# Kernel tuning notes

Measured on AMD Instinct MI355X. Metric: run time of the kernel, lower is better.

The kernel has to match this reference:

```python
import jax, jax.numpy as jnp
import numpy as np
from jax import lax

N, T, IN = 64, 1024, 64
H = 512
H2 = H // 2   # 256
H4 = H // 4   # 128
H10 = H // 10 # 51


def _lstm(x, Wih, Whh, bih, bhh):
    """PyTorch-style LSTM, batch_first. x: [N,T,in]. Returns hs [N,T,h], h_T, c_T."""
    n, t, _ = x.shape
    h = Whh.shape[1]
    b = bih + bhh

    def step(carry, xt):
        hprev, cprev = carry
        gates = xt @ Wih.T + hprev @ Whh.T + b
        i, f, g, o = jnp.split(gates, 4, axis=-1)
        i = jax.nn.sigmoid(i)
        f = jax.nn.sigmoid(f)
        g = jnp.tanh(g)
        o = jax.nn.sigmoid(o)
        c = f * cprev + i * g
        hnew = o * jnp.tanh(c)
        return (hnew, c), hnew

    h0 = jnp.zeros((n, h), x.dtype)
    c0 = jnp.zeros((n, h), x.dtype)
    (hT, cT), hs = lax.scan(step, (h0, c0), x.transpose(1, 0, 2))
    return hs.transpose(1, 0, 2), hT, cT


def _causal_self_attention(hs):
    """Unscaled dot-product causal attention, equivalent to the python loop."""
    n, t, h = hs.shape
    scores = jnp.einsum('nth,nsh->nts', hs, hs)  # [N,T,T]
    mask = jnp.tril(jnp.ones((t, t), bool))
    scores = jnp.where(mask[None], scores, -jnp.inf)
    attn = jax.nn.softmax(scores, axis=-1)
    return jnp.einsum('nts,nsh->nth', attn, hs)


def setup_inputs() -> dict:
    key = jax.random.key(0)
    ks = jax.random.split(key, 16)
    s = 0.05
    return {
        'x': jax.random.normal(ks[0], (N, T, IN), jnp.float32),
        'W_ih1': jax.random.normal(ks[1], (4 * H, IN), jnp.float32) * s,
        'W_hh1': jax.random.normal(ks[2], (4 * H, H), jnp.float32) * s,
        'b_ih1': jax.random.normal(ks[3], (4 * H,), jnp.float32) * s,
        'b_hh1': jax.random.normal(ks[4], (4 * H,), jnp.float32) * s,
        'W_ih2': jax.random.normal(ks[5], (4 * H2, H), jnp.float32) * s,
        'W_hh2': jax.random.normal(ks[6], (4 * H2, H2), jnp.float32) * s,
        'b_ih2': jax.random.normal(ks[7], (4 * H2,), jnp.float32) * s,
        'b_hh2': jax.random.normal(ks[8], (4 * H2,), jnp.float32) * s,
        'fc1_w': jax.random.normal(ks[9], (H4, 2 * H2), jnp.float32) * s,
        'fc1_b': jax.random.normal(ks[10], (H4,), jnp.float32) * s,
        'fc2_w': jax.random.normal(ks[11], (H10, H4), jnp.float32) * s,
        'fc2_b': jax.random.normal(ks[12], (H10,), jnp.float32) * s,
        'fc3_w': jax.random.normal(ks[13], (1, H10), jnp.float32) * s,
        'fc3_b': jax.random.normal(ks[14], (1,), jnp.float32) * s,
    }


def reference(x, W_ih1, W_hh1, b_ih1, b_hh1, W_ih2, W_hh2, b_ih2, b_hh2,
              fc1_w, fc1_b, fc2_w, fc2_b, fc3_w, fc3_b):
    out, h1, c1 = _lstm(x, W_ih1, W_hh1, b_ih1, b_hh1)     # [N,T,H]
    out, h2, c2 = _lstm(out, W_ih2, W_hh2, b_ih2, b_hh2)   # [N,T,H2]
    contexts = _causal_self_attention(out)                  # [N,T,H2]
    out = jnp.concatenate((contexts, out), axis=2)          # [N,T,2*H2]
    out = jax.nn.relu(out @ fc1_w.T + fc1_b)                # dropout_ratio=0 -> identity
    out = jax.nn.relu(out @ fc2_w.T + fc2_b)
    out = out @ fc3_w.T + fc3_b                              # [N,T,1]
    return out, h1, c1, h2, c2
```

## Files before the change

kernel.cpp:

```cpp
#include <hip/hip_runtime.h>
#include <hip/hip_bf16.h>

#define N_   64
#define T_   1024
#define IN_  64
#define H1_  512
#define H2_  256
#define NG   4
#define NU1  16
#define NU2  8
#define RING 8
#define RING2 4
#define SENT 0xAAAAAAAAu

typedef __bf16 bf16x8 __attribute__((ext_vector_type(8)));
typedef float  f32x4  __attribute__((ext_vector_type(4)));
typedef unsigned int u32x4 __attribute__((ext_vector_type(4)));
typedef unsigned short u16x8 __attribute__((ext_vector_type(8)));
typedef unsigned long long u64;
typedef __hip_bfloat16 bf16_t;

#define OFF_FLG2  8192u
#define OFF_QUE   12288u
#define ZERO_BYTES 16384u
#define OFF_H1R   16384u
#define OFF_H2R   540672u
#define OFF_XB    671744u
#define OFF_W1    9060352u
#define OFF_W2    11419648u
#define OFF_B1    12992512u
#define OFF_B2    13000704u
#define OFF_FC1W  13004800u
#define OFF_FC2W  13135872u
#define OFF_HS2   13152256u
#define OFF_BURN  46706688u

__device__ __forceinline__ bf16x8 ld16(const bf16_t* p) {
  u32x4 u = *reinterpret_cast<const u32x4*>(p);
  return __builtin_bit_cast(bf16x8, u);
}
__device__ __forceinline__ u64 ld64_mall(const void* p) {
  return __hip_atomic_load((const u64*)p, __ATOMIC_RELAXED, __HIP_MEMORY_SCOPE_AGENT);
}
__device__ __forceinline__ void st4_mall(bf16_t* p, unsigned v) {
  __hip_atomic_store((unsigned*)p, v, __ATOMIC_RELAXED, __HIP_MEMORY_SCOPE_AGENT);
}
__device__ __forceinline__ unsigned ldflag(unsigned* p) {
  return __hip_atomic_load(p, __ATOMIC_RELAXED, __HIP_MEMORY_SCOPE_AGENT);
}
__device__ __forceinline__ bool sentok(u64 w) {
  return ((unsigned)w != SENT) && ((unsigned)(w >> 32) != SENT);
}
__device__ __forceinline__ f32x4 mfma_bf16(bf16x8 a, bf16x8 b, f32x4 c) {
  return __builtin_amdgcn_mfma_f32_16x16x32_bf16(a, b, c, 0, 0, 0);
}
__device__ __forceinline__ float sigf(float x) { return 1.f / (1.f + __expf(-x)); }
__device__ __forceinline__ float tanh_fast(float x) {
  float e = __expf(-2.f * fabsf(x));
  float r = (1.f - e) / (1.f + e);
  return x < 0.f ? -r : r;
}
__device__ __forceinline__ unsigned short bf16_bits(float v) {
  __hip_bfloat16 b = __float2bfloat16(v);
  return *reinterpret_cast<unsigned short*>(&b);
}

__global__ void setup_kernel(const float* __restrict__ x,
    const float* __restrict__ Wih1, const float* __restrict__ Whh1,
    const float* __restrict__ bih1, const float* __restrict__ bhh1,
    const float* __restrict__ Wih2, const float* __restrict__ Whh2,
    const float* __restrict__ bih2, const float* __restrict__ bhh2,
    const float* __restrict__ fc1w, const float* __restrict__ fc2w,
    char* __restrict__ ws)
{
  bf16_t* xb = (bf16_t*)(ws + OFF_XB);
  bf16_t* w1 = (bf16_t*)(ws + OFF_W1);
  bf16_t* w2 = (bf16_t*)(ws + OFF_W2);
  float*  b1 = (float*)(ws + OFF_B1);
  float*  b2 = (float*)(ws + OFF_B2);
  bf16_t* f1 = (bf16_t*)(ws + OFF_FC1W);
  bf16_t* f2 = (bf16_t*)(ws + OFF_FC2W);
  const long E0 = 4194304, E1 = E0 + 1179648, E2 = E1 + 786432,
             E3 = E2 + 2048, E4 = E3 + 1024, E5 = E4 + 65536, E6 = E5 + 8192;
  for (long i = blockIdx.x * (long)blockDim.x + threadIdx.x; i < E6;
       i += (long)gridDim.x * blockDim.x) {
    if (i < E0) {
      xb[i] = __float2bfloat16(x[i]);
    } else if (i < E1) {
      long idx = i - E0; long j = idx / 576, k = idx % 576;
      float v = (k < 64) ? Wih1[j * 64 + k] : Whh1[j * 512 + (k - 64)];
      w1[idx] = __float2bfloat16(v);
    } else if (i < E2) {
      long idx = i - E1; long j = idx / 768, k = idx % 768;
      float v = (k < 512) ? Wih2[j * 512 + k] : Whh2[j * 256 + (k - 512)];
      w2[idx] = __float2bfloat16(v);
    } else if (i < E3) {
      long idx = i - E2; b1[idx] = bih1[idx] + bhh1[idx];
    } else if (i < E4) {
      long idx = i - E3; b2[idx] = bih2[idx] + bhh2[idx];
    } else if (i < E5) {
      long idx = i - E4; f1[idx] = __float2bfloat16(fc1w[idx]);
    } else {
      long idx = i - E5; long j = idx / 128, k = idx % 128;
      f2[idx] = __float2bfloat16(j < 51 ? fc2w[j * 128 + k] : 0.f);
    }
  }
}

__global__ __launch_bounds__(256, 1) void fused_kernel(char* __restrict__ ws,
    const float* __restrict__ fc1b, const float* __restrict__ fc2b,
    const float* __restrict__ fc3w, const float* __restrict__ fc3b,
    float* __restrict__ dout)
{
  const bf16_t* xb  = (const bf16_t*)(ws + OFF_XB);
  const bf16_t* W1  = (const bf16_t*)(ws + OFF_W1);
  const bf16_t* W2  = (const bf16_t*)(ws + OFF_W2);
  const float*  b1  = (const float*)(ws + OFF_B1);
  const float*  b2  = (const float*)(ws + OFF_B2);
  bf16_t* h1r = (bf16_t*)(ws + OFF_H1R);
  bf16_t* h2r = (bf16_t*)(ws + OFF_H2R);
  bf16_t* hs2 = (bf16_t*)(ws + OFF_HS2);
  unsigned* flag2 = (unsigned*)(ws + OFF_FLG2);

  __shared__ __align__(16) char smem[55296];

  const int tid  = threadIdx.x;
  const int wave = tid >> 6;
  const int lane = tid & 63;
  const int l15  = lane & 15;
  const int quad = lane >> 4;
  const int bx   = blockIdx.x;
  const f32x4 z = {0.f, 0.f, 0.f, 0.f};

  if (bx < NG * NU1) {
    const int g = bx >> 4, u = bx & 15, u0 = u * 32;
    bf16_t* hstage = (bf16_t*)smem;
    float*  gbuf   = (float*)(smem + 18688);
    bf16x8 wf[18][2];
    #pragma unroll
    for (int i = 0; i < 18; ++i)
      #pragma unroll
      for (int nt = 0; nt < 2; ++nt)
        wf[i][nt] = ld16(W1 + (size_t)(wave * H1_ + u0 + nt * 16 + l15) * 576 + i * 32 + quad * 8);

    const int sr = tid >> 4;
    const int myp = tid & 15;
    const int row = tid >> 4, ui = (tid & 15) * 2;
    const int nrow = g * 16 + row;
    unsigned* bp = flag2 + (g * NU2 + (tid & 7)) * 32;
    float bi[2], bff[2], bg[2], bo[2], creg[2];
    #pragma unroll
    for (int j = 0; j < 2; ++j) {
      int ug = u0 + ui + j;
      bi[j]  = b1[ug];         bff[j] = b1[H1_ + ug];
      bg[j]  = b1[2*H1_ + ug]; bo[j]  = b1[3*H1_ + ug];
      creg[j] = 0.f;
    }
    #pragma unroll
    for (int s = 0; s < RING; ++s)
      st4_mall(h1r + ((size_t)(g * RING + s) * 16 + row) * 512 + u0 + ui, SENT);

    #pragma unroll 1
    for (int t = 0; t < T_; ++t) {
      {
        u64 xv = *(const u64*)(xb + ((size_t)(g*16 + sr) * T_ + t) * IN_ + myp * 4);
        *(u64*)(hstage + sr * 584 + myp * 4) = xv;
      }
      if (t >= 7)
        while ((int)ldflag(bp) < t - 6) __builtin_amdgcn_s_sleep(1);
      if (t == 0) {
        #pragma unroll
        for (int k = 0; k < 8; ++k)
          *(u64*)(hstage + sr * 584 + 64 + myp * 32 + k * 4) = 0ull;
      } else {
        const u64* src = (const u64*)(h1r + ((size_t)(g * RING + ((t-1) & 7)) * 16 + sr) * 512 + myp * 32);
        u64 w[8];
        for (;;) {
          #pragma unroll
          for (int k = 0; k < 8; ++k) w[k] = ld64_mall(src + k);
          bool ok = true;
          #pragma unroll
          for (int k = 0; k < 8; ++k) ok &= sentok(w[k]);
          if (ok) break;
          __builtin_amdgcn_s_sleep(1);
        }
        #pragma unroll
        for (int k = 0; k < 8; ++k)
          *(u64*)(hstage + sr * 584 + 64 + myp * 32 + k * 4) = w[k];
      }
      __syncthreads();
      st4_mall(h1r + ((size_t)(g * RING + ((t+1) & 7)) * 16 + row) * 512 + u0 + ui, SENT);
      f32x4 acc[2] = {z, z};
      #pragma unroll
      for (int ki = 0; ki < 18; ++ki) {
        bf16x8 aw = ld16(hstage + l15 * 584 + ki * 32 + quad * 8);
        acc[0] = mfma_bf16(aw, wf[ki][0], acc[0]);
        acc[1] = mfma_bf16(aw, wf[ki][1], acc[1]);
      }
      #pragma unroll
      for (int nt = 0; nt < 2; ++nt)
        #pragma unroll
        for (int r = 0; r < 4; ++r)
          gbuf[(wave * 16 + quad * 4 + r) * 33 + nt * 16 + l15] = acc[nt][r];
      __syncthreads();
      {
        unsigned pack = 0;
        float hv[2];
        #pragma unroll
        for (int j = 0; j < 2; ++j) {
          int col = ui + j;
          float iv = sigf(gbuf[(0*16 + row) * 33 + col] + bi[j]);
          float fv = sigf(gbuf[(1*16 + row) * 33 + col] + bff[j]);
          float gv = tanh_fast(gbuf[(2*16 + row) * 33 + col] + bg[j]);
          float ov = sigf(gbuf[(3*16 + row) * 33 + col] + bo[j]);
          float c = fv * creg[j] + iv * gv;
          creg[j] = c;
          float h = ov * tanh_fast(c);
          hv[j] = h;
          pack |= (unsigned)bf16_bits(h) << (16 * j);
        }
        st4_mall(h1r + ((size_t)(g * RING + (t & 7)) * 16 + row) * 512 + u0 + ui, pack);
        if (t == T_ - 1) {
          #pragma unroll
          for (int j = 0; j < 2; ++j) {
            dout[65536 + nrow * H1_ + u0 + ui + j] = hv[j];
            dout[98304 + nrow * H1_ + u0 + ui + j] = creg[j];
          }
        }
      }
    }
  } else if (bx < NG * NU1 + NG * NU2) {
    const int b2x = bx - NG * NU1;
    const int g = b2x >> 3, u = b2x & 7, u0 = u * 32;
    bf16_t* hstage = (bf16_t*)smem;
    float*  gbuf   = (float*)(smem + 25088);
    bf16x8 wf[24][2];
    #pragma unroll
    for (int i = 0; i < 24; ++i)
      #pragma unroll
      for (int nt = 0; nt < 2; ++nt)
        wf[i][nt] = ld16(W2 + (size_t)(wave * H2_ + u0 + nt * 16 + l15) * 768 + i * 32 + quad * 8);

    const int sr = tid >> 4;
    const int q  = tid & 15;
    const int row = tid >> 4, ui = (tid & 15) * 2;
    const int nrow = g * 16 + row;
    float bi[2], bff[2], bg[2], bo[2], creg[2];
    #pragma unroll
    for (int j = 0; j < 2; ++j) {
      int ug = u0 + ui + j;
      bi[j]  = b2[ug];         bff[j] = b2[H2_ + ug];
      bg[j]  = b2[2*H2_ + ug]; bo[j]  = b2[3*H2_ + ug];
      creg[j] = 0.f;
    }
    #pragma unroll
    for (int s = 0; s < RING2; ++s)
      st4_mall(h2r + ((size_t)(g * RING2 + s) * 16 + row) * 256 + u0 + ui, SENT);

    #pragma unroll 1
    for (int t = 0; t < T_; ++t) {
      {
        const u64* s1 = (const u64*)(h1r + ((size_t)(g * RING + (t & 7)) * 16 + sr) * 512 + q * 32);
        u64 w[8];
        for (;;) {
          #pragma unroll
          for (int k = 0; k < 8; ++k) w[k] = ld64_mall(s1 + k);
          bool ok = true;
          #pragma unroll
          for (int k = 0; k < 8; ++k) ok &= sentok(w[k]);
          if (ok) break;
          __builtin_amdgcn_s_sleep(1);
        }
        #pragma unroll
        for (int k = 0; k < 8; ++k)
          *(u64*)(hstage + sr * 784 + q * 32 + k * 4) = w[k];
      }
      if (t == 0) {
        #pragma unroll
        for (int k = 0; k < 4; ++k)
          *(u64*)(hstage + sr * 784 + 512 + q * 16 + k * 4) = 0ull;
      } else {
        const u64* s2 = (const u64*)(h2r + ((size_t)(g * RING2 + ((t-1) & 3)) * 16 + sr) * 256 + q * 16);
        u64 w[4];
        for (;;) {
          #pragma unroll
          for (int k = 0; k < 4; ++k) w[k] = ld64_mall(s2 + k);
          bool ok = true;
          #pragma unroll
          for (int k = 0; k < 4; ++k) ok &= sentok(w[k]);
          if (ok) break;
          __builtin_amdgcn_s_sleep(1);
        }
        #pragma unroll
        for (int k = 0; k < 4; ++k)
          *(u64*)(hstage + sr * 784 + 512 + q * 16 + k * 4) = w[k];
      }
      __syncthreads();
      st4_mall(h2r + ((size_t)(g * RING2 + ((t+1) & 3)) * 16 + row) * 256 + u0 + ui, SENT);
      f32x4 acc[2] = {z, z};
      #pragma unroll
      for (int ki = 0; ki < 24; ++ki) {
        bf16x8 aw = ld16(hstage + l15 * 784 + ki * 32 + quad * 8);
        acc[0] = mfma_bf16(aw, wf[ki][0], acc[0]);
        acc[1] = mfma_bf16(aw, wf[ki][1], acc[1]);
      }
      #pragma unroll
      for (int nt = 0; nt < 2; ++nt)
        #pragma unroll
        for (int r = 0; r < 4; ++r)
          gbuf[(wave * 16 + quad * 4 + r) * 33 + nt * 16 + l15] = acc[nt][r];
      __syncthreads();
      {
        unsigned pack = 0;
        float hv[2];
        #pragma unroll
        for (int j = 0; j < 2; ++j) {
          int col = ui + j;
          float iv = sigf(gbuf[(0*16 + row) * 33 + col] + bi[j]);
          float fv = sigf(gbuf[(1*16 + row) * 33 + col] + bff[j]);
          float gv = tanh_fast(gbuf[(2*16 + row) * 33 + col] + bg[j]);
          float ov = sigf(gbuf[(3*16 + row) * 33 + col] + bo[j]);
          float c = fv * creg[j] + iv * gv;
          creg[j] = c;
          float h = ov * tanh_fast(c);
          hv[j] = h;
          pack |= (unsigned)bf16_bits(h) << (16 * j);
        }
        st4_mall(h2r + ((size_t)(g * RING2 + (t & 3)) * 16 + row) * 256 + u0 + ui, pack);
        st4_mall(hs2 + ((size_t)nrow * T_ + t) * H2_ + u0 + ui, pack);
        if (t == T_ - 1) {
          #pragma unroll
          for (int j = 0; j < 2; ++j) {
            dout[131072 + nrow * H2_ + u0 + ui + j] = hv[j];
            dout[147456 + nrow * H2_ + u0 + ui + j] = creg[j];
          }
        }
      }
      __syncthreads();
      if (tid == 0)
        __hip_atomic_store(flag2 + (g * NU2 + u) * 32, (unsigned)(t + 1),
                           __ATOMIC_RELAXED, __HIP_MEMORY_SCOPE_AGENT);
    }
  }

  __syncthreads();
  {
    const bf16_t* f1w = (const bf16_t*)(ws + OFF_FC1W);
    const bf16_t* f2w = (const bf16_t*)(ws + OFF_FC2W);
    unsigned* queue = (unsigned*)(ws + OFF_QUE);
    unsigned short* vtile = (unsigned short*)smem;
    bf16_t* plds   = (bf16_t*)(smem + 36864);
    bf16_t* ctxlds = (bf16_t*)smem;
    bf16_t* act1   = (bf16_t*)(smem + 36864);
    float*  act2   = (float*)smem;
    volatile int* itemslot = (volatile int*)(smem + 55040);
    float burn = 1.0f;

    for (;;) {
      if (tid == 0) *itemslot = (int)atomicAdd(queue, 1u);
      __syncthreads();
      const int item = *itemslot;
      __syncthreads();
      if (item >= 1024) break;
      const int qt = item >> 6, n = item & 63, q0 = qt * 64, gg = n >> 4;

      {
        const int need = q0 + 64;
        if (tid < 64) {
          unsigned* p = (lane < NU2) ? flag2 + (gg * NU2 + lane) * 32 : nullptr;
          bool ok = (p == nullptr) || ((int)ldflag(p) >= need);
          while (!__all(ok)) {
            #pragma unroll
            for (int k = 0; k < 32; ++k) burn = fmaf(burn, 1.0000001f, 1e-7f);
            ok = (p == nullptr) || ((int)ldflag(p) >= need);
          }
        }
        __syncthreads();
      }

      bf16x8 aq[8];
      #pragma unroll
      for (int ks = 0; ks < 8; ++ks)
        aq[ks] = ld16(hs2 + ((size_t)n * T_ + q0 + wave * 16 + l15) * H2_ + ks * 32 + quad * 8);
      f32x4 o[16];
      #pragma unroll
      for (int ct = 0; ct < 16; ++ct) o[ct] = z;
      float m_run[4], l_run[4];
      #pragma unroll
      for (int r = 0; r < 4; ++r) { m_run[r] = -1e30f; l_run[r] = 0.f; }
      bf16_t* pw = plds + wave * 1152;

      #pragma unroll 1
      for (int st = 0; st <= qt; ++st) {
        const int s0 = st * 64;
        __syncthreads();
        #pragma unroll
        for (int it = 0; it < 8; ++it) {
          int s  = (tid >> 3) + (it & 1) * 32;
          int c0 = (tid & 7) * 8 + (it >> 1) * 64;
          u16x8 v = *reinterpret_cast<const u16x8*>(
              (const unsigned short*)hs2 + ((size_t)n * T_ + s0 + s) * H2_ + c0);
          #pragma unroll
          for (int j = 0; j < 8; ++j) {
            int ch = c0 + j;
            int sw = (s & 7) | ((((s >> 3) ^ (ch >> 3)) & 7) << 3);
            vtile[ch * 72 + sw] = v[j];
          }
        }
        __syncthreads();
        f32x4 sc[4] = {z, z, z, z};
        #pragma unroll
        for (int ks = 0; ks < 8; ++ks) {
          #pragma unroll
          for (int nt = 0; nt < 4; ++nt) {
            bf16x8 bk = ld16(hs2 + ((size_t)n * T_ + s0 + nt * 16 + l15) * H2_ + ks * 32 + quad * 8);
            sc[nt] = mfma_bf16(aq[ks], bk, sc[nt]);
          }
        }
        if (st == qt) {
          int qg = q0 + wave * 16 + quad * 4;
          #pragma unroll
          for (int nt = 0; nt < 4; ++nt) {
            int sg = s0 + nt * 16 + l15;
            #pragma unroll
            for (int r = 0; r < 4; ++r)
              if (sg > qg + r) sc[nt][r] = -1e30f;
          }
        }
        float alpha[4];
        #pragma unroll
        for (int r = 0; r < 4; ++r) {
          float tm = fmaxf(fmaxf(sc[0][r], sc[1][r]), fmaxf(sc[2][r], sc[3][r]));
          tm = fmaxf(tm, __shfl_xor(tm, 1, 16));
          tm = fmaxf(tm, __shfl_xor(tm, 2, 16));
          tm = fmaxf(tm, __shfl_xor(tm, 4, 16));
          tm = fmaxf(tm, __shfl_xor(tm, 8, 16));
          float mnew = fmaxf(m_run[r], tm);
          alpha[r] = __expf(m_run[r] - mnew);
          m_run[r] = mnew;
          float ts = 0.f;
          #pragma unroll
          for (int nt = 0; nt < 4; ++nt) {
            float p = __expf(sc[nt][r] - mnew);
            sc[nt][r] = p;
            ts += p;
          }
          ts += __shfl_xor(ts, 1, 16);
          ts += __shfl_xor(ts, 2, 16);
          ts += __shfl_xor(ts, 4, 16);
          ts += __shfl_xor(ts, 8, 16);
          l_run[r] = l_run[r] * alpha[r] + ts;
        }
        #pragma unroll
        for (int ct = 0; ct < 16; ++ct)
          #pragma unroll
          for (int r = 0; r < 4; ++r)
            o[ct][r] *= alpha[r];
        #pragma unroll
        for (int nt = 0; nt < 4; ++nt)
          #pragma unroll
          for (int r = 0; r < 4; ++r)
            pw[(quad * 4 + r) * 72 + nt * 16 + l15] = __float2bfloat16(sc[nt][r]);
        #pragma unroll
        for (int ks2 = 0; ks2 < 2; ++ks2) {
          bf16x8 ap = ld16(pw + l15 * 72 + ks2 * 32 + quad * 8);
          #pragma unroll
          for (int ct = 0; ct < 16; ++ct) {
            int ch = ct * 16 + l15;
            int blk = ((ks2 * 4 + quad) ^ (ch >> 3)) & 7;
            bf16x8 bv = ld16((bf16_t*)vtile + ch * 72 + blk * 8);
            o[ct] = mfma_bf16(ap, bv, o[ct]);
          }
        }
      }
      __syncthreads();
      float inv[4];
      #pragma unroll
      for (int r = 0; r < 4; ++r) inv[r] = 1.f / l_run[r];
      #pragma unroll
      for (int ct = 0; ct < 16; ++ct)
        #pragma unroll
        for (int r = 0; r < 4; ++r)
          ctxlds[(wave * 16 + quad * 4 + r) * 264 + ct * 16 + l15] =
              __float2bfloat16(o[ct][r] * inv[r]);
      __syncthreads();

      f32x4 a1[4][2];
      #pragma unroll
      for (int mt = 0; mt < 4; ++mt) { a1[mt][0] = z; a1[mt][1] = z; }
      #pragma unroll
      for (int ks = 0; ks < 16; ++ks) {
        bf16x8 af[4];
        if (ks < 8) {
          #pragma unroll
          for (int mt = 0; mt < 4; ++mt)
            af[mt] = ld16(ctxlds + (mt * 16 + l15) * 264 + ks * 32 + quad * 8);
        } else {
          #pragma unroll
          for (int mt = 0; mt < 4; ++mt)
            af[mt] = ld16(hs2 + ((size_t)n * T_ + q0 + mt * 16 + l15) * H2_ + (ks - 8) * 32 + quad * 8);
        }
        #pragma unroll
        for (int nt = 0; nt < 2; ++nt) {
          bf16x8 bw = ld16(f1w + (size_t)(wave * 32 + nt * 16 + l15) * 512 + ks * 32 + quad * 8);
          #pragma unroll
          for (int mt = 0; mt < 4; ++mt)
            a1[mt][nt] = mfma_bf16(af[mt], bw, a1[mt][nt]);
        }
      }
      #pragma unroll
      for (int mt = 0; mt < 4; ++mt)
        #pragma unroll
        for (int nt = 0; nt < 2; ++nt)
          #pragma unroll
          for (int r = 0; r < 4; ++r) {
            int ch = wave * 32 + nt * 16 + l15;
            float v = a1[mt][nt][r] + fc1b[ch];
            act1[(mt * 16 + quad * 4 + r) * 136 + ch] = __float2bfloat16(fmaxf(v, 0.f));
          }
      __syncthreads();

      f32x4 a2[4] = {z, z, z, z};
      #pragma unroll
      for (int ks = 0; ks < 4; ++ks) {
        bf16x8 bw = ld16(f2w + (wave * 16 + l15) * 128 + ks * 32 + quad * 8);
        #pragma unroll
        for (int mt = 0; mt < 4; ++mt) {
          bf16x8 af = ld16(act1 + (mt * 16 + l15) * 136 + ks * 32 + quad * 8);
          a2[mt] = mfma_bf16(af, bw, a2[mt]);
        }
      }
      __syncthreads();
      #pragma unroll
      for (int mt = 0; mt < 4; ++mt)
        #pragma unroll
        for (int r = 0; r < 4; ++r) {
          int ch = wave * 16 + l15;
          int rw = mt * 16 + quad * 4 + r;
          float v = a2[mt][r] + (ch < 51 ? fc2b[ch] : 0.f);
          act2[rw * 68 + ch] = fmaxf(v, 0.f);
        }
      __syncthreads();
      if (tid < 64) {
        float s = fc3b[0];
        for (int c = 0; c < 51; ++c) s += act2[tid * 68 + c] * fc3w[c];
        dout[(size_t)n * T_ + q0 + tid] = s;
      }
      __syncthreads();
    }
    if (burn == 0.1234567f)
      ((float*)(ws + OFF_BURN))[tid] = burn;
  }
}

extern "C" void kernel_launch(void* const* d_in, const int* in_sizes, int n_in,
                              void* d_out, int out_size, void* d_ws, size_t ws_size,
                              hipStream_t stream) {
  (void)in_sizes; (void)n_in; (void)out_size; (void)ws_size;
  const float* x    = (const float*)d_in[0];
  const float* Wih1 = (const float*)d_in[1];
  const float* Whh1 = (const float*)d_in[2];
  const float* bih1 = (const float*)d_in[3];
  const float* bhh1 = (const float*)d_in[4];
  const float* Wih2 = (const float*)d_in[5];
  const float* Whh2 = (const float*)d_in[6];
  const float* bih2 = (const float*)d_in[7];
  const float* bhh2 = (const float*)d_in[8];
  const float* fc1w = (const float*)d_in[9];
  const float* fc1b = (const float*)d_in[10];
  const float* fc2w = (const float*)d_in[11];
  const float* fc2b = (const float*)d_in[12];
  const float* fc3w = (const float*)d_in[13];
  const float* fc3b = (const float*)d_in[14];
  char* ws  = (char*)d_ws;
  float* out = (float*)d_out;

  hipMemsetAsync(ws, 0, ZERO_BYTES, stream);
  setup_kernel<<<2048, 256, 0, stream>>>(x, Wih1, Whh1, bih1, bhh1,
                                         Wih2, Whh2, bih2, bhh2, fc1w, fc2w, ws);
  fused_kernel<<<256, 256, 0, stream>>>(ws, fc1b, fc2b, fc3w, fc3b, out);
}
```

Measured before the change: 3.182 ms.

## Prefetch next h1 slice, split MFMA chains, drop spin sleeps, move flag publish

Layer-2 blocks now speculatively load the next timestep's h1 ring slice at the end of each step and only re-poll if sentinels are still present. The flag2 publish moves to right after the staging barrier, signalling step t-1 consumed, and the trailing __syncthreads per step is removed. Both LSTM layers split the MFMA accumulation into two independent chains to cut dependency latency, and the s_sleep in spin loops is dropped to react faster. The changes shorten the serial per-step critical path. In exchange, the sleep-free spinning adds memory traffic, and the reordered flag and barrier protocol risks ring-reuse races.

```diff
diff --git a/kernel.cpp b/kernel.cpp
--- a/kernel.cpp
+++ b/kernel.cpp
@@ -182,7 +182,6 @@
           #pragma unroll
           for (int k = 0; k < 8; ++k) ok &= sentok(w[k]);
           if (ok) break;
-          __builtin_amdgcn_s_sleep(1);
         }
         #pragma unroll
         for (int k = 0; k < 8; ++k)
@@ -190,13 +189,20 @@
       }
       __syncthreads();
       st4_mall(h1r + ((size_t)(g * RING + ((t+1) & 7)) * 16 + row) * 512 + u0 + ui, SENT);
-      f32x4 acc[2] = {z, z};
-      #pragma unroll
-      for (int ki = 0; ki < 18; ++ki) {
+      f32x4 acc[2] = {z, z}, acd[2] = {z, z};
+      #pragma unroll
+      for (int ki = 0; ki < 9; ++ki) {
         bf16x8 aw = ld16(hstage + l15 * 584 + ki * 32 + quad * 8);
         acc[0] = mfma_bf16(aw, wf[ki][0], acc[0]);
         acc[1] = mfma_bf16(aw, wf[ki][1], acc[1]);
       }
+      #pragma unroll
+      for (int ki = 9; ki < 18; ++ki) {
+        bf16x8 aw = ld16(hstage + l15 * 584 + ki * 32 + quad * 8);
+        acd[0] = mfma_bf16(aw, wf[ki][0], acd[0]);
+        acd[1] = mfma_bf16(aw, wf[ki][1], acd[1]);
+      }
+      acc[0] += acd[0]; acc[1] += acd[1];
       #pragma unroll
       for (int nt = 0; nt < 2; ++nt)
         #pragma unroll
@@ -245,6 +251,7 @@
     const int q  = tid & 15;
     const int row = tid >> 4, ui = (tid & 15) * 2;
     const int nrow = g * 16 + row;
+    unsigned* myflag = flag2 + (g * NU2 + u) * 32;
     float bi[2], bff[2], bg[2], bo[2], creg[2];
     #pragma unroll
     for (int j = 0; j < 2; ++j) {
@@ -257,23 +264,29 @@
     for (int s = 0; s < RING2; ++s)
       st4_mall(h2r + ((size_t)(g * RING2 + s) * 16 + row) * 256 + u0 + ui, SENT);
 
+    u64 pf[8];
     #pragma unroll 1
     for (int t = 0; t < T_; ++t) {
       {
         const u64* s1 = (const u64*)(h1r + ((size_t)(g * RING + (t & 7)) * 16 + sr) * 512 + q * 32);
-        u64 w[8];
-        for (;;) {
-          #pragma unroll
-          for (int k = 0; k < 8; ++k) w[k] = ld64_mall(s1 + k);
-          bool ok = true;
-          #pragma unroll
-          for (int k = 0; k < 8; ++k) ok &= sentok(w[k]);
-          if (ok) break;
-          __builtin_amdgcn_s_sleep(1);
+        bool good = (t > 0);
+        if (good) {
+          #pragma unroll
+          for (int k = 0; k < 8; ++k) good &= sentok(pf[k]);
+        }
+        if (!good) {
+          for (;;) {
+            #pragma unroll
+            for (int k = 0; k < 8; ++k) pf[k] = ld64_mall(s1 + k);
+            bool ok = true;
+            #pragma unroll
+            for (int k = 0; k < 8; ++k) ok &= sentok(pf[k]);
+            if (ok) break;
+          }
         }
         #pragma unroll
         for (int k = 0; k < 8; ++k)
-          *(u64*)(hstage + sr * 784 + q * 32 + k * 4) = w[k];
+          *(u64*)(hstage + sr * 784 + q * 32 + k * 4) = pf[k];
       }
       if (t == 0) {
         #pragma unroll
@@ -289,21 +302,29 @@
           #pragma unroll
           for (int k = 0; k < 4; ++k) ok &= sentok(w[k]);
           if (ok) break;
-          __builtin_amdgcn_s_sleep(1);
         }
         #pragma unroll
         for (int k = 0; k < 4; ++k)
           *(u64*)(hstage + sr * 784 + 512 + q * 16 + k * 4) = w[k];
       }
       __syncthreads();
+      if (tid == 0 && t > 0)
+        __hip_atomic_store(myflag, (unsigned)t, __ATOMIC_RELAXED, __HIP_MEMORY_SCOPE_AGENT);
       st4_mall(h2r + ((size_t)(g * RING2 + ((t+1) & 3)) * 16 + row) * 256 + u0 + ui, SENT);
-      f32x4 acc[2] = {z, z};
-      #pragma unroll
-      for (int ki = 0; ki < 24; ++ki) {
+      f32x4 acc[2] = {z, z}, acd[2] = {z, z};
+      #pragma unroll
+      for (int ki = 0; ki < 12; ++ki) {
         bf16x8 aw = ld16(hstage + l15 * 784 + ki * 32 + quad * 8);
         acc[0] = mfma_bf16(aw, wf[ki][0], acc[0]);
         acc[1] = mfma_bf16(aw, wf[ki][1], acc[1]);
       }
+      #pragma unroll
+      for (int ki = 12; ki < 24; ++ki) {
+        bf16x8 aw = ld16(hstage + l15 * 784 + ki * 32 + quad * 8);
+        acd[0] = mfma_bf16(aw, wf[ki][0], acd[0]);
+        acd[1] = mfma_bf16(aw, wf[ki][1], acd[1]);
+      }
+      acc[0] += acd[0]; acc[1] += acd[1];
       #pragma unroll
       for (int nt = 0; nt < 2; ++nt)
         #pragma unroll
@@ -336,11 +357,15 @@
           }
         }
       }
-      __syncthreads();
-      if (tid == 0)
-        __hip_atomic_store(flag2 + (g * NU2 + u) * 32, (unsigned)(t + 1),
-                           __ATOMIC_RELAXED, __HIP_MEMORY_SCOPE_AGENT);
+      if (t + 1 < T_) {
+        const u64* nx = (const u64*)(h1r + ((size_t)(g * RING + ((t+1) & 7)) * 16 + sr) * 512 + q * 32);
+        #pragma unroll
+        for (int k = 0; k < 8; ++k) pf[k] = ld64_mall(nx + k);
+      }
     }
+    __syncthreads();
+    if (tid == 0)
+      __hip_atomic_store(myflag, (unsigned)T_, __ATOMIC_RELAXED, __HIP_MEMORY_SCOPE_AGENT);
   }
 
   __syncthreads();
```

Result: faster. 3.108 ms (-2.3%).
